# Performance work log

Hardware: AMD Instinct MI355X
Metric: run time of the kernel (lower is better)

Reference implementation:

```python
import jax, jax.numpy as jnp
import numpy as np

S, B, D, H, HD = 2048, 4, 1280, 16, 80  # seq, batch, d_model, heads, head_dim
NSEG = 8


def setup_inputs() -> dict:
    key = jax.random.key(0)
    k0, k1, k2 = jax.random.split(key, 3)
    x = jax.random.normal(k0, (S, B, D), dtype=jnp.float32)
    Wqkv = jax.random.normal(k1, (D, 3 * D), dtype=jnp.float32) * 0.02
    bqkv = jnp.zeros((3 * D,), dtype=jnp.float32)
    Wproj = jax.random.normal(k2, (D, 4 * D), dtype=jnp.float32) * 0.02
    bproj = jnp.zeros((4 * D,), dtype=jnp.float32)
    # 8 equal windows of 256 tokens: [0, 256, 512, ..., 2048]
    cu_seqlens = (jnp.arange(NSEG + 1, dtype=jnp.int32) * (S // NSEG))
    return {"x": x, "Wqkv": Wqkv, "bqkv": bqkv, "Wproj": Wproj,
            "bproj": bproj, "cu_seqlens": cu_seqlens}


def reference(x, Wqkv, bqkv, Wproj, bproj, cu_seqlens):
    s, b, d = x.shape
    qkv = x @ Wqkv + bqkv                     # [s, b, 3d]
    q, k, v = jnp.split(qkv, 3, axis=2)       # each [s, b, d]
    def to_bhsd(t):
        return t.reshape(s, b, H, HD).transpose(1, 2, 0, 3)  # [b, h, s, hd]
    q, k, v = to_bhsd(q), to_bhsd(k), to_bhsd(v)
    # Block-diagonal mask: token t belongs to window searchsorted(cu[1:], t, right)
    pos = jnp.arange(s)
    seg = jnp.searchsorted(cu_seqlens[1:], pos, side='right')  # [s]
    bias = jnp.where(seg[:, None] == seg[None, :], 0.0,
                     jnp.finfo(x.dtype).min)                   # [s, s]
    scale = 1.0 / jnp.sqrt(jnp.asarray(HD, dtype=x.dtype))
    scores = jnp.einsum('bhsd,bhtd->bhst', q, k) * scale + bias
    attn = jax.nn.softmax(scores, axis=-1)
    out = jnp.einsum('bhst,bhtd->bhsd', attn, v)               # [b, h, s, hd]
    context = out.transpose(2, 0, 1, 3).reshape(s, b, H * HD)  # [s, b, d]
    return context @ Wproj + bproj                             # [s, b, 4d]
```

## Files before the change

### kernel.cpp

```cpp
#include <hip/hip_runtime.h>

typedef _Float16 f16;
typedef _Float16 f16x8 __attribute__((ext_vector_type(8)));
typedef _Float16 f16x4 __attribute__((ext_vector_type(4)));
typedef float    f32x4 __attribute__((ext_vector_type(4)));
typedef unsigned int u32t;

#define AS1 __attribute__((address_space(1)))
#define AS3 __attribute__((address_space(3)))

static __device__ __forceinline__ void gload_lds16(const void* g, void* l) {
  __builtin_amdgcn_global_load_lds((const AS1 u32t*)g, (AS3 u32t*)l, 16, 0, 0);
}

static __device__ __forceinline__ f16x8 zero8() {
  f16x8 z;
#pragma unroll
  for (int j = 0; j < 8; ++j) z[j] = (f16)0;
  return z;
}

__global__ void k_cvt_x(const float* __restrict__ in, f16* __restrict__ out, int n4) {
  int stride = gridDim.x * blockDim.x;
  for (int i = blockIdx.x * blockDim.x + threadIdx.x; i < n4; i += stride) {
    float4 v = ((const float4*)in)[i];
    f16x4 o;
    o[0] = (f16)v.x; o[1] = (f16)v.y; o[2] = (f16)v.z; o[3] = (f16)v.w;
    ((f16x4*)out)[i] = o;
  }
}

__global__ void k_cvt_w_t(const float* __restrict__ W, f16* __restrict__ Wt, int N) {
  __shared__ float T[32][33];
  int bk = blockIdx.x % 40;
  int bn = blockIdx.x / 40;
  int k0 = bk * 32, n0 = bn * 32;
  int r = threadIdx.x >> 5;
  int c = threadIdx.x & 31;
#pragma unroll
  for (int i = 0; i < 4; ++i)
    T[r + i * 8][c] = W[(size_t)(k0 + r + i * 8) * N + n0 + c];
  __syncthreads();
#pragma unroll
  for (int i = 0; i < 4; ++i)
    Wt[(size_t)(n0 + r + i * 8) * 1280 + k0 + c] = (f16)T[c][r + i * 8];
}


template<int NCOLS, bool F16OUT>
__global__ __launch_bounds__(512, 2)
void gemm_nt(const f16* __restrict__ A, const f16* __restrict__ Bt,
             const float* __restrict__ bias, void* __restrict__ Cout)
{
  __shared__ __align__(16) char lds[131072];
  const int tid = threadIdx.x;
  const int wave = tid >> 6, lane = tid & 63;
  const int rl = lane & 15, g = lane >> 4;
  const int wm = wave >> 2, wn = wave & 3;

  constexpr int NBN = NCOLS / 256;
  constexpr int NWG = 32 * NBN;
  const int bid = blockIdx.x;
  const int wgid = (bid & 7) * (NWG / 8) + (bid >> 3);
  const int bm = wgid / NBN, bn = wgid % NBN;
  const long row0 = (long)bm * 256, col0 = (long)bn * 256;

  const int srow = tid >> 3;
  const int scol = ((tid & 7) ^ (srow & 7)) << 4;
  const char* gA = (const char*)A  + (row0 + srow) * 2560 + scol;
  const char* gB = (const char*)Bt + (col0 + srow) * 2560 + scol;
  char* const ldsw = lds + wave * 1024;

  auto STAGE4 = [&](int tk, int buf) {
    const long kb = (long)tk * 128;
#pragma unroll
    for (int half = 0; half < 2; ++half) {
      const char* sa = gA + half * (128 * 2560) + kb;
      char* da = ldsw + buf * 65536 + half * 16384;
      gload_lds16(sa, da);
      gload_lds16(sa + 64 * 2560, da + 8192);
      const char* sb = gB + half * (128 * 2560) + kb;
      char* db = ldsw + buf * 65536 + 32768 + half * 16384;
      gload_lds16(sb, db);
      gload_lds16(sb + 64 * 2560, db + 8192);
    }
  };

  const int swz0 = ((0 + g) ^ (rl & 7)) << 4;
  const int swz1 = ((4 + g) ^ (rl & 7)) << 4;
  const int aoff = (wm * 128 + rl) << 7;
  const int boff = 32768 + ((wn * 64 + rl) << 7);

  auto LDA = [&](f16x8 (&af)[8], int buf, int mh) {
#pragma unroll
    for (int m = 0; m < 4; ++m) {
      const char* p = lds + buf * 65536 + aoff + (mh * 4 + m) * 2048;
      af[m * 2 + 0] = *(const f16x8*)(p + swz0);
      af[m * 2 + 1] = *(const f16x8*)(p + swz1);
    }
  };
  auto LDB = [&](f16x8 (&bf)[4], int buf, int nh) {
#pragma unroll
    for (int n = 0; n < 2; ++n) {
      const char* p = lds + buf * 65536 + boff + (nh * 2 + n) * 2048;
      bf[n * 2 + 0] = *(const f16x8*)(p + swz0);
      bf[n * 2 + 1] = *(const f16x8*)(p + swz1);
    }
  };

  f32x4 acc[8][4];
#pragma unroll
  for (int m = 0; m < 8; ++m)
#pragma unroll
    for (int n = 0; n < 4; ++n) acc[m][n] = (f32x4){0.f, 0.f, 0.f, 0.f};

  auto MM = [&](int mh, int nh, const f16x8 (&af)[8], const f16x8 (&bf)[4]) {
    __builtin_amdgcn_s_setprio(1);
#pragma unroll
    for (int m = 0; m < 4; ++m)
#pragma unroll
      for (int n = 0; n < 2; ++n)
#pragma unroll
        for (int kk = 0; kk < 2; ++kk)
          acc[mh * 4 + m][nh * 2 + n] = __builtin_amdgcn_mfma_f32_16x16x32_f16(
              af[m * 2 + kk], bf[n * 2 + kk], acc[mh * 4 + m][nh * 2 + n], 0, 0, 0);
    __builtin_amdgcn_s_setprio(0);
  };

  auto TILEBODY = [&](int buf, int stk) {
    if (stk >= 0) STAGE4(stk, buf ^ 1);
    f16x8 afL[8], afH[8], bf0[4], bf1[4];
    LDA(afL, buf, 0);
    LDB(bf0, buf, 0);
    LDB(bf1, buf, 1);
    MM(0, 0, afL, bf0);
    MM(0, 1, afL, bf1);
    LDA(afH, buf, 1);
    MM(1, 1, afH, bf1);
    MM(1, 0, afH, bf0);
  };

  STAGE4(0, 0);
  __syncthreads();

#pragma unroll 1
  for (int tp = 0; tp < 10; ++tp) {
    TILEBODY(0, 2 * tp + 1);
    __syncthreads();
    TILEBODY(1, tp < 9 ? 2 * tp + 2 : -1);
    __syncthreads();
  }

#pragma unroll
  for (int m = 0; m < 8; ++m) {
#pragma unroll
    for (int n = 0; n < 4; ++n) {
      long c = col0 + wn * 64 + n * 16 + rl;
      float bv = bias[c];
#pragma unroll
      for (int r = 0; r < 4; ++r) {
        long rr = row0 + wm * 128 + m * 16 + g * 4 + r;
        float v = acc[m][n][r] + bv;
        if (F16OUT) ((f16*)Cout)[rr * NCOLS + c] = (f16)v;
        else        ((float*)Cout)[rr * NCOLS + c] = v;
      }
    }
  }
}

__global__ void k_vt(const f16* __restrict__ qkv, f16* __restrict__ vt) {
  __shared__ __align__(16) f16 T[128 * 136];
  int bid = blockIdx.x;
  int sc16 = bid & 15, bh = bid >> 4;
  int b = bh >> 4, h = bh & 15;
  int s0 = sc16 * 128;
  int t = threadIdx.x;
#pragma unroll
  for (int i = 0; i < 5; ++i) {
    int cid = i * 256 + t;
    int s = cid / 10, c = cid % 10;
    const f16* g = qkv + (size_t)((s0 + s) * 4 + b) * 3840 + 2560 + h * 80 + c * 8;
    f16x8 v = *(const f16x8*)g;
    int phys = c ^ ((s >> 3) & 7);
    *(f16x8*)(T + s * 136 + phys * 8) = v;
  }
  __syncthreads();
#pragma unroll
  for (int i = 0; i < 5; ++i) {
    int oid = i * 256 + t;
    int sc8 = oid & 15, hd = oid >> 4;
    f16x8 o;
#pragma unroll
    for (int j = 0; j < 8; ++j) {
      int row = sc8 * 8 + j;
      int phys = (hd >> 3) ^ (sc8 & 7);
      o[j] = T[row * 136 + phys * 8 + (hd & 7)];
    }
    *(f16x8*)(vt + (size_t)(bh * 80 + hd) * 2048 + s0 + sc8 * 8) = o;
  }
}

__global__ __launch_bounds__(512, 2)
void k_attn(const f16* __restrict__ qkv, const f16* __restrict__ vt,
            f16* __restrict__ ctx)
{
  __shared__ __align__(16) f16 sK[256 * 104];
  __shared__ __align__(16) f16 sV[80 * 264];
  __shared__ __align__(16) f16 sP[128 * 72];

  const int bid = blockIdx.x;
  const int qc = bid & 1, seg = (bid >> 1) & 7, h = (bid >> 4) & 15, b = bid >> 8;
  const int t = threadIdx.x;
  const int wave = t >> 6, lane = t & 63;
  const int s_key0 = seg * 256;

#pragma unroll
  for (int i = 0; i < 5; ++i) {
    int cid = i * 512 + t;
    int key = cid / 10, c = cid % 10;
    const f16* g = qkv + (size_t)((s_key0 + key) * 4 + b) * 3840 + 1280 + h * 80 + c * 8;
    *(f16x8*)(sK + key * 104 + c * 8) = *(const f16x8*)g;
  }
  {
    int key = t >> 1, c = t & 1;
    *(f16x8*)(sK + key * 104 + 80 + c * 8) = zero8();
  }
#pragma unroll
  for (int i = 0; i < 5; ++i) {
    int cid = i * 512 + t;
    int hd = cid >> 5, c = cid & 31;
    const f16* g = vt + (size_t)((b * 16 + h) * 80 + hd) * 2048 + s_key0 + c * 8;
    *(f16x8*)(sV + hd * 264 + c * 8) = *(const f16x8*)g;
  }

  const int q0 = s_key0 + qc * 128 + wave * 16;
  const int rl = lane & 15, g = lane >> 4;
  f16x8 qf[3];
  {
    const f16* gq = qkv + (size_t)((q0 + rl) * 4 + b) * 3840 + h * 80;
    qf[0] = *(const f16x8*)(gq + g * 8);
    qf[1] = *(const f16x8*)(gq + 32 + g * 8);
    if (g < 2) qf[2] = *(const f16x8*)(gq + 64 + g * 8);
    else       qf[2] = zero8();
  }
  __syncthreads();

  f32x4 sc[16];
#pragma unroll
  for (int nt = 0; nt < 16; ++nt) sc[nt] = (f32x4){0.f, 0.f, 0.f, 0.f};
#pragma unroll
  for (int nt = 0; nt < 16; ++nt) {
#pragma unroll
    for (int kk = 0; kk < 3; ++kk) {
      f16x8 bf = *(const f16x8*)(sK + (nt * 16 + rl) * 104 + kk * 32 + g * 8);
      sc[nt] = __builtin_amdgcn_mfma_f32_16x16x32_f16(qf[kk], bf, sc[nt], 0, 0, 0);
    }
  }

  const float scale = 0.11180339887498949f;
  float inv[4];
#pragma unroll
  for (int r = 0; r < 4; ++r) {
    float m = -1e30f;
#pragma unroll
    for (int nt = 0; nt < 16; ++nt) m = fmaxf(m, sc[nt][r]);
#pragma unroll
    for (int off = 8; off >= 1; off >>= 1) m = fmaxf(m, __shfl_xor(m, off));
    m *= scale;
    float sum = 0.f;
#pragma unroll
    for (int nt = 0; nt < 16; ++nt) {
      float p = __expf(sc[nt][r] * scale - m);
      sc[nt][r] = p;
      sum += p;
    }
#pragma unroll
    for (int off = 8; off >= 1; off >>= 1) sum += __shfl_xor(sum, off);
    inv[r] = 1.0f / sum;
  }

  f32x4 o[5];
#pragma unroll
  for (int nt = 0; nt < 5; ++nt) o[nt] = (f32x4){0.f, 0.f, 0.f, 0.f};
  const int prow0 = wave * 16;
  for (int ch = 0; ch < 4; ++ch) {
#pragma unroll
    for (int f = 0; f < 4; ++f) {
      int nt = ch * 4 + f;
#pragma unroll
      for (int r = 0; r < 4; ++r)
        sP[(prow0 + g * 4 + r) * 72 + f * 16 + rl] = (f16)sc[nt][r];
    }
#pragma unroll
    for (int kk = 0; kk < 2; ++kk) {
      f16x8 pa = *(const f16x8*)(sP + (prow0 + rl) * 72 + kk * 32 + g * 8);
#pragma unroll
      for (int nt = 0; nt < 5; ++nt) {
        f16x8 vb = *(const f16x8*)(sV + (nt * 16 + rl) * 264 + ch * 64 + kk * 32 + g * 8);
        o[nt] = __builtin_amdgcn_mfma_f32_16x16x32_f16(pa, vb, o[nt], 0, 0, 0);
      }
    }
  }

#pragma unroll
  for (int nt = 0; nt < 5; ++nt) {
    int hd = nt * 16 + rl;
#pragma unroll
    for (int r = 0; r < 4; ++r) {
      long qrow = q0 + g * 4 + r;
      float v = o[nt][r] * inv[r];
      ctx[(qrow * 4 + b) * 1280 + h * 80 + hd] = (f16)v;
    }
  }
}

extern "C" void kernel_launch(void* const* d_in, const int* in_sizes, int n_in,
                              void* d_out, int out_size, void* d_ws, size_t ws_size,
                              hipStream_t stream)
{
  const float* x     = (const float*)d_in[0];
  const float* Wqkv  = (const float*)d_in[1];
  const float* bqkv  = (const float*)d_in[2];
  const float* Wproj = (const float*)d_in[3];
  const float* bproj = (const float*)d_in[4];

  char* ws = (char*)d_ws;
  f16* X16   = (f16*)(ws);
  f16* WQT   = (f16*)(ws + 20971520);
  f16* WPT   = (f16*)(ws + 30801920);
  f16* QKV16 = (f16*)(ws + 43909120);
  f16* VT    = (f16*)(ws + 106823680);
  f16* CTX16 = X16;

  k_cvt_x<<<4096, 256, 0, stream>>>(x, X16, 8192 * 1280 / 4);
  k_cvt_w_t<<<40 * 120, 256, 0, stream>>>(Wqkv, WQT, 3840);
  k_cvt_w_t<<<40 * 160, 256, 0, stream>>>(Wproj, WPT, 5120);
  gemm_nt<3840, true ><<<480, 512, 0, stream>>>(X16, WQT, bqkv, QKV16);
  k_vt<<<1024, 256, 0, stream>>>(QKV16, VT);
  k_attn<<<1024, 512, 0, stream>>>(QKV16, VT, CTX16);
  gemm_nt<5120, false><<<640, 512, 0, stream>>>(CTX16, WPT, bproj, d_out);
}
```

Before: 281.6 us.

## Pipeline GEMM loads at quarter-tile granularity and double query rows per attention block

The GEMM main loop is restructured so global-to-LDS loads are issued per half-tile of A and B and interleaved between the four MFMA quadrants, with explicit barriers and vmcnt/lgkmcnt waits replacing whole-tile staging and __syncthreads. Launch bounds drop to one block per CU, which raises the register budget. Separately, the attention kernel now has each wave handle 32 query rows, so one block covers a full 256-token window and K/V are loaded once instead of twice, with half as many blocks launched. The risks are lower occupancy, higher register pressure in attention, and fragile hand-tuned wait counts.

```diff
diff --git a/kernel.cpp b/kernel.cpp
--- a/kernel.cpp
+++ b/kernel.cpp
@@ -48,7 +48,7 @@
 
 
 template<int NCOLS, bool F16OUT>
-__global__ __launch_bounds__(512, 2)
+__global__ __launch_bounds__(512, 1)
 void gemm_nt(const f16* __restrict__ A, const f16* __restrict__ Bt,
              const float* __restrict__ bias, void* __restrict__ Cout)
 {
@@ -65,36 +65,37 @@
   const int bm = wgid / NBN, bn = wgid % NBN;
   const long row0 = (long)bm * 256, col0 = (long)bn * 256;
 
-  const int srow = tid >> 3;
-  const int scol = ((tid & 7) ^ (srow & 7)) << 4;
-  const char* gA = (const char*)A  + (row0 + srow) * 2560 + scol;
-  const char* gB = (const char*)Bt + (col0 + srow) * 2560 + scol;
-  char* const ldsw = lds + wave * 1024;
-
-  auto STAGE4 = [&](int tk, int buf) {
-    const long kb = (long)tk * 128;
-#pragma unroll
-    for (int half = 0; half < 2; ++half) {
-      const char* sa = gA + half * (128 * 2560) + kb;
-      char* da = ldsw + buf * 65536 + half * 16384;
-      gload_lds16(sa, da);
-      gload_lds16(sa + 64 * 2560, da + 8192);
-      const char* sb = gB + half * (128 * 2560) + kb;
-      char* db = ldsw + buf * 65536 + 32768 + half * 16384;
-      gload_lds16(sb, db);
-      gload_lds16(sb + 64 * 2560, db + 8192);
-    }
+  const int subA = wave * 8 + (lane >> 3);
+  const int cpA  = (((lane & 7) ^ (subA & 7)) << 4);
+  const char* gAt = (const char*)A + (row0 + subA) * 2560 + cpA;
+  const int subB = (wave & 3) * 8 + (lane >> 3);
+  const int cpB  = (((lane & 7) ^ (subB & 7)) << 4);
+  const char* gBt = (const char*)Bt + (col0 + (wave >> 2) * 64 + subB) * 2560 + cpB;
+  char* const dA = lds + wave * 1024;
+  char* const dB = lds + 65536 + wave * 1024;
+
+  auto STA = [&](int mh, int buf, int kb) {
+#pragma unroll
+    for (int l = 0; l < 2; ++l)
+      gload_lds16(gAt + mh * (64 * 2560) + l * (128 * 2560) + kb,
+                  dA + buf * 32768 + mh * 16384 + l * 8192);
+  };
+  auto STB = [&](int nh, int buf, int kb) {
+#pragma unroll
+    for (int l = 0; l < 2; ++l)
+      gload_lds16(gBt + nh * (32 * 2560) + l * (128 * 2560) + kb,
+                  dB + buf * 32768 + nh * 16384 + l * 8192);
   };
 
   const int swz0 = ((0 + g) ^ (rl & 7)) << 4;
   const int swz1 = ((4 + g) ^ (rl & 7)) << 4;
-  const int aoff = (wm * 128 + rl) << 7;
-  const int boff = 32768 + ((wn * 64 + rl) << 7);
+  const int aro = wm * 8192 + rl * 128;
+  const int bro = 65536 + wn * 4096 + rl * 128;
 
   auto LDA = [&](f16x8 (&af)[8], int buf, int mh) {
 #pragma unroll
     for (int m = 0; m < 4; ++m) {
-      const char* p = lds + buf * 65536 + aoff + (mh * 4 + m) * 2048;
+      const char* p = lds + buf * 32768 + mh * 16384 + aro + m * 2048;
       af[m * 2 + 0] = *(const f16x8*)(p + swz0);
       af[m * 2 + 1] = *(const f16x8*)(p + swz1);
     }
@@ -102,7 +103,7 @@
   auto LDB = [&](f16x8 (&bf)[4], int buf, int nh) {
 #pragma unroll
     for (int n = 0; n < 2; ++n) {
-      const char* p = lds + buf * 65536 + boff + (nh * 2 + n) * 2048;
+      const char* p = lds + buf * 32768 + nh * 16384 + bro + n * 2048;
       bf[n * 2 + 0] = *(const f16x8*)(p + swz0);
       bf[n * 2 + 1] = *(const f16x8*)(p + swz1);
     }
@@ -127,29 +128,43 @@
     __builtin_amdgcn_s_setprio(0);
   };
 
-  auto TILEBODY = [&](int buf, int stk) {
-    if (stk >= 0) STAGE4(stk, buf ^ 1);
-    f16x8 afL[8], afH[8], bf0[4], bf1[4];
-    LDA(afL, buf, 0);
-    LDB(bf0, buf, 0);
+#define BAR()   do { __builtin_amdgcn_s_barrier(); asm volatile("" ::: "memory"); } while (0)
+#define WLGKM() asm volatile("s_waitcnt lgkmcnt(0)" ::: "memory")
+#define WVM(N)  asm volatile("s_waitcnt vmcnt(" #N ")" ::: "memory")
+
+  auto TILE = [&](int buf, int kbB1, int kbN, int mode) {
+    f16x8 af[8], bf0[4], bf1[4];
+    LDA(af, buf, 0); LDB(bf0, buf, 0);
+    if (mode <= 1) STB(1, buf ^ 1, kbB1);
+    BAR(); WLGKM(); MM(0, 0, af, bf0); BAR();
     LDB(bf1, buf, 1);
-    MM(0, 0, afL, bf0);
-    MM(0, 1, afL, bf1);
-    LDA(afH, buf, 1);
-    MM(1, 1, afH, bf1);
-    MM(1, 0, afH, bf0);
-  };
-
-  STAGE4(0, 0);
-  __syncthreads();
+    if (mode == 0) STA(0, buf, kbN);
+    BAR(); WLGKM(); MM(0, 1, af, bf1); BAR();
+    LDA(af, buf, 1);
+    if (mode == 0) STB(0, buf, kbN);
+    BAR(); WLGKM(); MM(1, 1, af, bf1); BAR();
+    if (mode == 0) STA(1, buf, kbN);
+    if (mode == 0) { WVM(6); } else if (mode == 1) { WVM(0); }
+    BAR(); MM(1, 0, af, bf0);
+    if (mode != 2) BAR();
+  };
+
+  STA(0, 0, 0); STB(0, 0, 0); STA(1, 0, 0); STB(1, 0, 0);
+  STA(0, 1, 128); STB(0, 1, 128); STA(1, 1, 128);
+  WVM(6); BAR();
 
 #pragma unroll 1
-  for (int tp = 0; tp < 10; ++tp) {
-    TILEBODY(0, 2 * tp + 1);
-    __syncthreads();
-    TILEBODY(1, tp < 9 ? 2 * tp + 2 : -1);
-    __syncthreads();
-  }
+  for (int it = 0; it < 9; ++it) {
+    const int kb = it * 256;
+    TILE(0, kb + 128, kb + 256, 0);
+    TILE(1, kb + 256, kb + 384, 0);
+  }
+  TILE(0, 2432, 0, 1);
+  TILE(1, 0, 0, 2);
+
+#undef BAR
+#undef WLGKM
+#undef WVM
 
 #pragma unroll
   for (int m = 0; m < 8; ++m) {
@@ -206,10 +221,10 @@
 {
   __shared__ __align__(16) f16 sK[256 * 104];
   __shared__ __align__(16) f16 sV[80 * 264];
-  __shared__ __align__(16) f16 sP[128 * 72];
+  __shared__ __align__(16) f16 sP[256 * 72];
 
   const int bid = blockIdx.x;
-  const int qc = bid & 1, seg = (bid >> 1) & 7, h = (bid >> 4) & 15, b = bid >> 8;
+  const int seg = bid & 7, h = (bid >> 3) & 15, b = bid >> 7;
   const int t = threadIdx.x;
   const int wave = t >> 6, lane = t & 63;
   const int s_key0 = seg * 256;
@@ -233,71 +248,80 @@
     *(f16x8*)(sV + hd * 264 + c * 8) = *(const f16x8*)g;
   }
 
-  const int q0 = s_key0 + qc * 128 + wave * 16;
+  const int q0 = s_key0 + wave * 32;
   const int rl = lane & 15, g = lane >> 4;
-  f16x8 qf[3];
+  f16x8 qfl[3], qfh[3];
   {
-    const f16* gq = qkv + (size_t)((q0 + rl) * 4 + b) * 3840 + h * 80;
-    qf[0] = *(const f16x8*)(gq + g * 8);
-    qf[1] = *(const f16x8*)(gq + 32 + g * 8);
-    if (g < 2) qf[2] = *(const f16x8*)(gq + 64 + g * 8);
-    else       qf[2] = zero8();
+    const f16* gl = qkv + (size_t)((q0 + rl) * 4 + b) * 3840 + h * 80;
+    const f16* gh = qkv + (size_t)((q0 + 16 + rl) * 4 + b) * 3840 + h * 80;
+    qfl[0] = *(const f16x8*)(gl + g * 8);
+    qfh[0] = *(const f16x8*)(gh + g * 8);
+    qfl[1] = *(const f16x8*)(gl + 32 + g * 8);
+    qfh[1] = *(const f16x8*)(gh + 32 + g * 8);
+    if (g < 2) { qfl[2] = *(const f16x8*)(gl + 64 + g * 8); qfh[2] = *(const f16x8*)(gh + 64 + g * 8); }
+    else       { qfl[2] = zero8(); qfh[2] = zero8(); }
   }
   __syncthreads();
 
-  f32x4 sc[16];
-#pragma unroll
-  for (int nt = 0; nt < 16; ++nt) sc[nt] = (f32x4){0.f, 0.f, 0.f, 0.f};
+  f32x4 scl[16], sch[16];
+#pragma unroll
+  for (int nt = 0; nt < 16; ++nt) { scl[nt] = (f32x4){0.f,0.f,0.f,0.f}; sch[nt] = (f32x4){0.f,0.f,0.f,0.f}; }
 #pragma unroll
   for (int nt = 0; nt < 16; ++nt) {
 #pragma unroll
     for (int kk = 0; kk < 3; ++kk) {
       f16x8 bf = *(const f16x8*)(sK + (nt * 16 + rl) * 104 + kk * 32 + g * 8);
-      sc[nt] = __builtin_amdgcn_mfma_f32_16x16x32_f16(qf[kk], bf, sc[nt], 0, 0, 0);
+      scl[nt] = __builtin_amdgcn_mfma_f32_16x16x32_f16(qfl[kk], bf, scl[nt], 0, 0, 0);
+      sch[nt] = __builtin_amdgcn_mfma_f32_16x16x32_f16(qfh[kk], bf, sch[nt], 0, 0, 0);
     }
   }
 
   const float scale = 0.11180339887498949f;
-  float inv[4];
+  float invl[4], invh[4];
 #pragma unroll
   for (int r = 0; r < 4; ++r) {
-    float m = -1e30f;
-#pragma unroll
-    for (int nt = 0; nt < 16; ++nt) m = fmaxf(m, sc[nt][r]);
-#pragma unroll
-    for (int off = 8; off >= 1; off >>= 1) m = fmaxf(m, __shfl_xor(m, off));
-    m *= scale;
-    float sum = 0.f;
+    float ml = -1e30f, mh = -1e30f;
+#pragma unroll
+    for (int nt = 0; nt < 16; ++nt) { ml = fmaxf(ml, scl[nt][r]); mh = fmaxf(mh, sch[nt][r]); }
+#pragma unroll
+    for (int off = 8; off >= 1; off >>= 1) { ml = fmaxf(ml, __shfl_xor(ml, off)); mh = fmaxf(mh, __shfl_xor(mh, off)); }
+    ml *= scale; mh *= scale;
+    float suml = 0.f, sumh = 0.f;
 #pragma unroll
     for (int nt = 0; nt < 16; ++nt) {
-      float p = __expf(sc[nt][r] * scale - m);
-      sc[nt][r] = p;
-      sum += p;
-    }
-#pragma unroll
-    for (int off = 8; off >= 1; off >>= 1) sum += __shfl_xor(sum, off);
-    inv[r] = 1.0f / sum;
-  }
-
-  f32x4 o[5];
-#pragma unroll
-  for (int nt = 0; nt < 5; ++nt) o[nt] = (f32x4){0.f, 0.f, 0.f, 0.f};
-  const int prow0 = wave * 16;
+      float pl = __expf(scl[nt][r] * scale - ml);
+      float ph = __expf(sch[nt][r] * scale - mh);
+      scl[nt][r] = pl; sch[nt][r] = ph;
+      suml += pl; sumh += ph;
+    }
+#pragma unroll
+    for (int off = 8; off >= 1; off >>= 1) { suml += __shfl_xor(suml, off); sumh += __shfl_xor(sumh, off); }
+    invl[r] = 1.0f / suml; invh[r] = 1.0f / sumh;
+  }
+
+  f32x4 ol[5], oh[5];
+#pragma unroll
+  for (int nt = 0; nt < 5; ++nt) { ol[nt] = (f32x4){0.f,0.f,0.f,0.f}; oh[nt] = (f32x4){0.f,0.f,0.f,0.f}; }
+  const int prow0 = wave * 32;
   for (int ch = 0; ch < 4; ++ch) {
 #pragma unroll
     for (int f = 0; f < 4; ++f) {
       int nt = ch * 4 + f;
 #pragma unroll
-      for (int r = 0; r < 4; ++r)
-        sP[(prow0 + g * 4 + r) * 72 + f * 16 + rl] = (f16)sc[nt][r];
+      for (int r = 0; r < 4; ++r) {
+        sP[(prow0 + g * 4 + r) * 72 + f * 16 + rl]      = (f16)scl[nt][r];
+        sP[(prow0 + 16 + g * 4 + r) * 72 + f * 16 + rl] = (f16)sch[nt][r];
+      }
     }
 #pragma unroll
     for (int kk = 0; kk < 2; ++kk) {
-      f16x8 pa = *(const f16x8*)(sP + (prow0 + rl) * 72 + kk * 32 + g * 8);
+      f16x8 pal = *(const f16x8*)(sP + (prow0 + rl) * 72 + kk * 32 + g * 8);
+      f16x8 pah = *(const f16x8*)(sP + (prow0 + 16 + rl) * 72 + kk * 32 + g * 8);
 #pragma unroll
       for (int nt = 0; nt < 5; ++nt) {
         f16x8 vb = *(const f16x8*)(sV + (nt * 16 + rl) * 264 + ch * 64 + kk * 32 + g * 8);
-        o[nt] = __builtin_amdgcn_mfma_f32_16x16x32_f16(pa, vb, o[nt], 0, 0, 0);
+        ol[nt] = __builtin_amdgcn_mfma_f32_16x16x32_f16(pal, vb, ol[nt], 0, 0, 0);
+        oh[nt] = __builtin_amdgcn_mfma_f32_16x16x32_f16(pah, vb, oh[nt], 0, 0, 0);
       }
     }
   }
@@ -307,9 +331,10 @@
     int hd = nt * 16 + rl;
 #pragma unroll
     for (int r = 0; r < 4; ++r) {
-      long qrow = q0 + g * 4 + r;
-      float v = o[nt][r] * inv[r];
-      ctx[(qrow * 4 + b) * 1280 + h * 80 + hd] = (f16)v;
+      long qrl = q0 + g * 4 + r;
+      ctx[(qrl * 4 + b) * 1280 + h * 80 + hd] = (f16)(ol[nt][r] * invl[r]);
+      long qrh = q0 + 16 + g * 4 + r;
+      ctx[(qrh * 4 + b) * 1280 + h * 80 + hd] = (f16)(oh[nt][r] * invh[r]);
     }
   }
 }
@@ -337,6 +362,6 @@
   k_cvt_w_t<<<40 * 160, 256, 0, stream>>>(Wproj, WPT, 5120);
   gemm_nt<3840, true ><<<480, 512, 0, stream>>>(X16, WQT, bqkv, QKV16);
   k_vt<<<1024, 256, 0, stream>>>(QKV16, VT);
-  k_attn<<<1024, 512, 0, stream>>>(QKV16, VT, CTX16);
+  k_attn<<<512, 512, 0, stream>>>(QKV16, VT, CTX16);
   gemm_nt<5120, false><<<640, 512, 0, stream>>>(CTX16, WPT, bproj, d_out);
 }
```

Measured after the change: 271.8 us. 1.04x faster.
